# Optimization experiments

Hardware: AMD Instinct MI355X
Metric: run time of the kernel (lower is better)

Reference implementation:

```python
import jax, jax.numpy as jnp
import numpy as np

BN_EPS = 1e-5

def setup_inputs() -> dict:
    key = jax.random.key(0)
    ks = jax.random.split(key, 13)
    bs, ch, hei, wei = 4, 32, 32, 128  # n_features = wei = 128, ch = n_features//4
    nf = wei
    def p(k, shape, s=0.05):
        return jax.random.normal(k, shape, dtype=jnp.float32) * s
    return {
        "head": jax.random.normal(ks[0], (bs, ch, hei, wei), dtype=jnp.float32),
        "tail": jax.random.normal(ks[1], (bs, ch, hei, wei), dtype=jnp.float32),
        "R_q": p(ks[2], (nf, nf)), "R_k": p(ks[3], (nf, nf)),
        "R_v": p(ks[4], (nf, nf)), "R_W": p(ks[5], (nf, nf)),
        "F_q": p(ks[6], (nf, nf)), "F_k": p(ks[7], (nf, nf)),
        "F_v": p(ks[8], (nf, nf)), "F_W": p(ks[9], (nf, nf)),
        "conv_w": p(ks[10], (2, 2 * ch, 1, 1)),
        "conv_b": jnp.zeros((2,), jnp.float32),
        "bn_w": jnp.ones((2,), jnp.float32),
        "bn_b": jnp.zeros((2,), jnp.float32),
        "bn_mean": jnp.zeros((2,), jnp.float32),
        "bn_var": jnp.ones((2,), jnp.float32),
        "flag": 1,
    }

def _affinity(head, tail, conv_w, conv_b, bn_w, bn_b, bn_mean, bn_var):
    # 1x1 conv -> eval-mode BatchNorm2d -> ReLU -> softmax over channel dim
    x = jnp.concatenate([head, tail], axis=1)                       # [b,2c,h,w]
    a = jnp.einsum('bchw,oc->bohw', x, conv_w[:, :, 0, 0]) + conv_b[None, :, None, None]
    scale = (bn_w / jnp.sqrt(bn_var + BN_EPS))[None, :, None, None]
    a = (a - bn_mean[None, :, None, None]) * scale + bn_b[None, :, None, None]
    a = jax.nn.relu(a)
    return jax.nn.softmax(a, axis=1)                                # torch legacy dim=1 for 4D

def reference(head, tail, R_q, R_k, R_v, R_W, F_q, F_k, F_v, F_W,
              conv_w, conv_b, bn_w, bn_b, bn_mean, bn_var, flag):
    bs, ch, hei, wei = head.shape
    L = hei * wei
    ic = ch  # inter_channels == ch by construction
    aff = _affinity(head, tail, conv_w, conv_b, bn_w, bn_b, bn_mean, bn_var)
    if flag:
        alpha = aff[:, 0].reshape(bs, L, 1)                          # broadcast over last axis
        q = (head @ R_q).reshape(bs, ic, L).transpose(0, 2, 1)       # [b,L,ic]
        t_k = (tail @ F_k).reshape(bs, ic, L).transpose(0, 2, 1)     # [b,L,ic]
        t_v = (tail @ F_v).reshape(bs, ic, L)                        # [b,ic,L]
        f_t = t_k @ t_v                                              # [b,L,L]
        h_k = (head @ R_k).reshape(bs, ic, L).transpose(0, 2, 1)
        h_v = (head @ R_v).reshape(bs, ic, L)
        f_h = h_k @ h_v                                              # [b,L,L]
        att = jax.nn.softmax(alpha * f_t + f_h, axis=-1)
        y = (att @ q).transpose(0, 2, 1).reshape(bs, ic, hei, wei)
        return y @ R_W + head
    else:
        alpha = aff[:, 1].reshape(bs, L, 1)
        q = (tail @ F_q).reshape(bs, ic, L).transpose(0, 2, 1)
        h_k = (head @ R_k).reshape(bs, ic, L).transpose(0, 2, 1)
        h_v = (head @ R_v).reshape(bs, ic, L)
        f_h = h_k @ h_v
        t_k = (tail @ F_k).reshape(bs, ic, L).transpose(0, 2, 1)
        t_v = (tail @ F_v).reshape(bs, ic, L)
        f_t = t_k @ t_v
        att = jax.nn.softmax(alpha * f_h + f_t, axis=-1)
        y = (att @ q).transpose(0, 2, 1).reshape(bs, ic, hei, wei)
        return y @ F_W + tail
```

## Files before the change

### kernel.cpp

```cpp
#include <hip/hip_runtime.h>
#include <hip/hip_bf16.h>
#include <stdint.h>

typedef unsigned short u16;
typedef unsigned int u32;
typedef __attribute__((ext_vector_type(8))) short short8;
typedef __attribute__((ext_vector_type(4))) short short4_t;
typedef __attribute__((ext_vector_type(4))) float f32x4;

#define MFMA16(A,B,C) __builtin_amdgcn_mfma_f32_16x16x32_bf16((A),(B),(C),0,0,0)
#define L2E 1.4426950408889634f

__device__ __forceinline__ u16 f2bf(float f) {
  u32 x = __float_as_uint(f);
  u32 r = x + 0x7fffu + ((x >> 16) & 1u);
  return (u16)(r >> 16);
}
__device__ __forceinline__ float bf2f(short v) {
  return __uint_as_float((u32)(u16)v << 16);
}
__device__ __forceinline__ u32 pack_bf2(float a, float b) {
  __hip_bfloat162 h = __float22bfloat162_rn(make_float2(a, b));
  u32 u; __builtin_memcpy(&u, &h, 4); return u;
}
__device__ __forceinline__ short8 mk_frag(u32 w0, u32 w1, u32 w2, u32 w3) {
  union { u32 u[4]; short8 s; } cv;
  cv.u[0] = w0; cv.u[1] = w1; cv.u[2] = w2; cv.u[3] = w3;
  return cv.s;
}

__global__ void kprep(const float* R_q, const float* R_k, const float* R_v,
                      const float* R_W, const float* F_q, const float* F_k,
                      const float* F_v, const float* F_W, const int* flagp,
                      u16* matT)
{
  int flag = *flagp;
  const float* S;
  int m = blockIdx.x;
  if (flag) {
    const float* s[6] = {R_q, R_k, R_v, F_k, F_v, R_W}; S = s[m];
  } else {
    const float* s[6] = {F_q, F_k, F_v, R_k, R_v, F_W}; S = s[m];
  }
  u16* dst = matT + m * 16384;
  int base = blockIdx.y * 2048;
  for (int idx = base + threadIdx.x; idx < base + 2048; idx += blockDim.x) {
    int k = idx >> 7, n = idx & 127;
    dst[n * 128 + k] = f2bf(S[idx]);
  }
}

__global__ __launch_bounds__(256) void kproj(const float* __restrict__ head,
    const float* __restrict__ tail, const u16* __restrict__ matT,
    const float* __restrict__ conv_w, const float* __restrict__ conv_b,
    const float* __restrict__ bn_w, const float* __restrict__ bn_b,
    const float* __restrict__ bn_mean, const float* __restrict__ bn_var,
    u16* __restrict__ qT, u16* __restrict__ KQ,
    u16* __restrict__ Vc, const int* __restrict__ flagp)
{
  __shared__ u16 lds_t[128][34];
  __shared__ float s_alpha[128];
  const int flag = *flagp;
  const float* X1 = flag ? head : tail;
  const float* X2 = flag ? tail : head;
  const int bh = blockIdx.x, g = blockIdx.y;
  const int b = bh >> 5, h = bh & 31;
  const float* src = (g < 3) ? X1 : X2;
  const u16* Bm = matT + g * 16384;
  const int tid = threadIdx.x, lane = tid & 63, wid = tid >> 6;
  const int lrow = lane & 15, lg = lane >> 4;
  const int rt = wid & 1, cbase = (wid >> 1) * 64;

  if (g == 3) {
    if (tid < 128) {
      int w = tid;
      const float* hp = head + ((size_t)b * 1024 + h) * 128 + w;
      const float* tp = tail + ((size_t)b * 1024 + h) * 128 + w;
      float a0 = 0.f, a1 = 0.f;
      for (int c = 0; c < 32; ++c) {
        float xh = hp[c * 4096];
        float xt = tp[c * 4096];
        a0 += xh * conv_w[c]      + xt * conv_w[32 + c];
        a1 += xh * conv_w[64 + c] + xt * conv_w[96 + c];
      }
      const float eps = 1e-5f;
      a0 += conv_b[0]; a1 += conv_b[1];
      a0 = (a0 - bn_mean[0]) * (bn_w[0] * rsqrtf(bn_var[0] + eps)) + bn_b[0];
      a1 = (a1 - bn_mean[1]) * (bn_w[1] * rsqrtf(bn_var[1] + eps)) + bn_b[1];
      a0 = fmaxf(a0, 0.f); a1 = fmaxf(a1, 0.f);
      float asel = flag ? a0 : a1, aoth = flag ? a1 : a0;
      s_alpha[w] = 1.f / (1.f + __expf(aoth - asel));
    }
    __syncthreads();
  }

  f32x4 acc[4] = {};
  const float* Arow = src + (((size_t)b * 32 + rt * 16 + lrow) * 32 + h) * 128;
  #pragma unroll
  for (int k0 = 0; k0 < 128; k0 += 32) {
    short8 af;
    const float* ap = Arow + k0 + lg * 8;
    #pragma unroll
    for (int j = 0; j < 8; ++j) af[j] = (short)f2bf(ap[j]);
    #pragma unroll
    for (int cc = 0; cc < 4; ++cc) {
      short8 bf = *reinterpret_cast<const short8*>(
          Bm + (cbase + cc * 16 + lrow) * 128 + k0 + lg * 8);
      acc[cc] = MFMA16(af, bf, acc[cc]);
    }
  }
  #pragma unroll
  for (int cc = 0; cc < 4; ++cc) {
    int n = cbase + cc * 16 + lrow;
    float asc = (g == 1) ? L2E : 1.f;
    if (g == 3) asc = s_alpha[n] * L2E;
    #pragma unroll
    for (int rr = 0; rr < 4; ++rr) {
      int c = rt * 16 + lg * 4 + rr;
      lds_t[n][c] = f2bf(acc[cc][rr] * asc);
    }
  }
  __syncthreads();
  if (g == 0) {
    int c = tid >> 3, w0 = (tid & 7) * 16;
    int tw[8];
    #pragma unroll
    for (int i2 = 0; i2 < 8; ++i2)
      tw[i2] = (int)lds_t[w0 + 2 * i2][c] | ((int)lds_t[w0 + 2 * i2 + 1][c] << 16);
    int4* dst = reinterpret_cast<int4*>(qT + ((size_t)b * 32 + c) * 4096 + h * 128 + w0);
    dst[0] = make_int4(tw[0], tw[1], tw[2], tw[3]);
    dst[1] = make_int4(tw[4], tw[5], tw[6], tw[7]);
  } else if (tid < 128) {
    int w = tid;
    int tw[16];
    #pragma unroll
    for (int i2 = 0; i2 < 16; ++i2)
      tw[i2] = (int)lds_t[w][2 * i2] | ((int)lds_t[w][2 * i2 + 1] << 16);
    u16* base = (g == 2 || g == 4) ? Vc : KQ;
    int coff = (g >= 3) ? 32 : 0;
    int4* dst = reinterpret_cast<int4*>(base + ((size_t)b * 4096 + h * 128 + w) * 64 + coff);
    dst[0] = make_int4(tw[0],  tw[1],  tw[2],  tw[3]);
    dst[1] = make_int4(tw[4],  tw[5],  tw[6],  tw[7]);
    dst[2] = make_int4(tw[8],  tw[9],  tw[10], tw[11]);
    dst[3] = make_int4(tw[12], tw[13], tw[14], tw[15]);
  }
}

__global__ __launch_bounds__(256, 6) void kattn(const u16* __restrict__ qT,
    const u16* __restrict__ KQ, const u16* __restrict__ Vc,
    u16* __restrict__ pO, float* __restrict__ pm, float* __restrict__ pl)
{
  __shared__ __align__(16) char lds_v[2][8192];
  __shared__ __align__(16) char lds_q[2][4096];
  const int b = blockIdx.y;
  const int i0 = blockIdx.x * 64;
  const int sp = blockIdx.z;
  const int jbase = sp * 512;
  const int tid = threadIdx.x, lane = tid & 63, wid = tid >> 6;
  const int lrow = lane & 15, lg = lane >> 4;

  const u16* KQb = KQ + (size_t)b * 4096 * 64;
  const u16* Vb  = Vc + (size_t)b * 4096 * 64;
  const u16* qTb = qT + (size_t)b * 32 * 4096;

  short8 bkq[2];
  {
    int r = i0 + wid * 16 + lrow;
    #pragma unroll
    for (int kc = 0; kc < 2; ++kc)
      bkq[kc] = *reinterpret_cast<const short8*>(KQb + (size_t)r * 64 + kc * 32 + lg * 8);
  }

  const int sr = tid >> 3, sx = (tid & 7) * 16;
  const int pr = (((sr >> 2) & 3) << 3) + (((sr >> 4) & 1) << 2) + (sr & 3);

  #pragma unroll
  for (int q = 0; q < 2; ++q) {
    int r = sr + q * 32, gr = pr + q * 32;
    int4 v = *reinterpret_cast<const int4*>(
        reinterpret_cast<const char*>(Vb + (size_t)(jbase + gr) * 64) + sx);
    *reinterpret_cast<int4*>(lds_v[0] + r * 128 + (sx ^ ((r & 7) << 4))) = v;
  }
  {
    int4 qv = *reinterpret_cast<const int4*>(
        qTb + (size_t)sr * 4096 + jbase + (tid & 7) * 8);
    *reinterpret_cast<int4*>(lds_q[0] + sr * 128 + (sx ^ ((sr & 7) << 4))) = qv;
  }
  __syncthreads();

  float m_run = -1e30f, l_run = 0.f;
  f32x4 accO[2] = {};
  int4 stgV[2], stgQ;

  for (int t = 0; t < 8; ++t) {
    const int buf = t & 1;
    if (t < 7) {
      const u16* Vn = Vb + (size_t)(jbase + (t + 1) * 64) * 64;
      #pragma unroll
      for (int q = 0; q < 2; ++q) {
        int gr = pr + q * 32;
        stgV[q] = *reinterpret_cast<const int4*>(
            reinterpret_cast<const char*>(Vn + (size_t)gr * 64) + sx);
      }
      stgQ = *reinterpret_cast<const int4*>(
          qTb + (size_t)sr * 4096 + jbase + (t + 1) * 64 + (tid & 7) * 8);
    }
    f32x4 st[4];
    __builtin_amdgcn_s_setprio(1);
    #pragma unroll
    for (int sub = 0; sub < 4; ++sub) {
      f32x4 a = {};
      #pragma unroll
      for (int kc = 0; kc < 2; ++kc) {
        int r = sub * 16 + lrow;
        int xs = kc * 64 + lg * 16;
        short8 av = *reinterpret_cast<const short8*>(
            lds_v[buf] + r * 128 + (xs ^ ((r & 7) << 4)));
        a = MFMA16(av, bkq[kc], a);
      }
      st[sub] = a;
    }
    __builtin_amdgcn_s_setprio(0);
    short8 aq[2][2];
    #pragma unroll
    for (int w = 0; w < 2; ++w)
      #pragma unroll
      for (int ct = 0; ct < 2; ++ct) {
        int r = ct * 16 + lrow;
        int xs = w * 64 + lg * 16;
        aq[w][ct] = *reinterpret_cast<const short8*>(
            lds_q[buf] + r * 128 + (xs ^ ((r & 7) << 4)));
      }
    float tm = -1e30f;
    #pragma unroll
    for (int sub = 0; sub < 4; ++sub)
      #pragma unroll
      for (int rr = 0; rr < 4; ++rr) tm = fmaxf(tm, st[sub][rr]);
    tm = fmaxf(tm, __shfl_xor(tm, 16, 64));
    tm = fmaxf(tm, __shfl_xor(tm, 32, 64));
    if (!__all((int)(tm <= m_run + 8.f))) {
      float m_new = fmaxf(m_run, tm);
      float scale = exp2f(m_run - m_new);
      l_run *= scale;
      #pragma unroll
      for (int ct = 0; ct < 2; ++ct)
        #pragma unroll
        for (int rr = 0; rr < 4; ++rr) accO[ct][rr] *= scale;
      m_run = m_new;
    }
    float ps = 0.f;
    #pragma unroll
    for (int sub = 0; sub < 4; ++sub)
      #pragma unroll
      for (int rr = 0; rr < 4; ++rr) {
        float p = exp2f(st[sub][rr] - m_run);
        st[sub][rr] = p;
        ps += p;
      }
    ps += __shfl_xor(ps, 16, 64);
    ps += __shfl_xor(ps, 32, 64);
    l_run += ps;

    __builtin_amdgcn_s_setprio(1);
    #pragma unroll
    for (int w = 0; w < 2; ++w) {
      short8 bp = mk_frag(pack_bf2(st[2 * w][0],     st[2 * w][1]),
                          pack_bf2(st[2 * w][2],     st[2 * w][3]),
                          pack_bf2(st[2 * w + 1][0], st[2 * w + 1][1]),
                          pack_bf2(st[2 * w + 1][2], st[2 * w + 1][3]));
      #pragma unroll
      for (int ct = 0; ct < 2; ++ct)
        accO[ct] = MFMA16(aq[w][ct], bp, accO[ct]);
    }
    __builtin_amdgcn_s_setprio(0);

    if (t < 7) {
      #pragma unroll
      for (int q = 0; q < 2; ++q) {
        int r = sr + q * 32;
        *reinterpret_cast<int4*>(lds_v[buf ^ 1] + r * 128 + (sx ^ ((r & 7) << 4))) = stgV[q];
      }
      *reinterpret_cast<int4*>(lds_q[buf ^ 1] + sr * 128 + (sx ^ ((sr & 7) << 4))) = stgQ;
      __syncthreads();
    }
  }

  const int i = i0 + wid * 16 + lrow;
  u16* pOb = pO + (size_t)((b * 8 + sp) * 32) * 4096;
  #pragma unroll
  for (int ct = 0; ct < 2; ++ct)
    #pragma unroll
    for (int rr = 0; rr < 4; ++rr)
      pOb[(size_t)(ct * 16 + lg * 4 + rr) * 4096 + i] = f2bf(accO[ct][rr]);
  if (lg == 0) {
    pm[(b * 8 + sp) * 4096 + i] = m_run;
    pl[(b * 8 + sp) * 4096 + i] = l_run;
  }
}

__global__ __launch_bounds__(128) void kout(const u16* __restrict__ pO,
    const float* __restrict__ pm, const float* __restrict__ pl,
    const u16* __restrict__ matT, const float* __restrict__ head,
    const float* __restrict__ tail, const int* __restrict__ flagp,
    float* __restrict__ out)
{
  __shared__ u16 ylds[16][136];
  const int flag = *flagp;
  const float* X1 = flag ? head : tail;
  const u16* Bm = matT + 5 * 16384;
  const int tid = threadIdx.x;
  const int rbase = blockIdx.x * 16;
  const int b = rbase >> 10, c = (rbase >> 5) & 31, h0 = rbase & 31;
  const int ioff = h0 * 128 + tid * 16;

  #pragma unroll
  for (int iq = 0; iq < 4; ++iq) {
    float4 msp[8];
    #pragma unroll
    for (int sp = 0; sp < 8; ++sp)
      msp[sp] = *reinterpret_cast<const float4*>(
          pm + (size_t)((b * 8 + sp) * 4096) + ioff + iq * 4);
    float4 M4 = msp[0];
    #pragma unroll
    for (int sp = 1; sp < 8; ++sp) {
      M4.x = fmaxf(M4.x, msp[sp].x); M4.y = fmaxf(M4.y, msp[sp].y);
      M4.z = fmaxf(M4.z, msp[sp].z); M4.w = fmaxf(M4.w, msp[sp].w);
    }
    float4 L4 = {0.f, 0.f, 0.f, 0.f}, y4 = {0.f, 0.f, 0.f, 0.f};
    #pragma unroll
    for (int sp = 0; sp < 8; ++sp) {
      float4 w4;
      w4.x = exp2f(msp[sp].x - M4.x); w4.y = exp2f(msp[sp].y - M4.y);
      w4.z = exp2f(msp[sp].z - M4.z); w4.w = exp2f(msp[sp].w - M4.w);
      float4 l4 = *reinterpret_cast<const float4*>(
          pl + (size_t)((b * 8 + sp) * 4096) + ioff + iq * 4);
      L4.x += w4.x * l4.x; L4.y += w4.y * l4.y;
      L4.z += w4.z * l4.z; L4.w += w4.w * l4.w;
      short4_t o4 = *reinterpret_cast<const short4_t*>(
          pO + (size_t)(((b * 8 + sp) * 32 + c)) * 4096 + ioff + iq * 4);
      y4.x += w4.x * bf2f(o4[0]); y4.y += w4.y * bf2f(o4[1]);
      y4.z += w4.z * bf2f(o4[2]); y4.w += w4.w * bf2f(o4[3]);
    }
    y4.x /= L4.x; y4.y /= L4.y; y4.z /= L4.z; y4.w /= L4.w;
    uint2 pk2;
    pk2.x = pack_bf2(y4.x, y4.y);
    pk2.y = pack_bf2(y4.z, y4.w);
    *reinterpret_cast<uint2*>(&ylds[tid >> 3][(tid & 7) * 16 + iq * 4]) = pk2;
  }
  __syncthreads();

  const int lane = tid & 63, wid = tid >> 6;
  const int lrow = lane & 15, lg = lane >> 4;
  const int ctbase = wid * 4;
  f32x4 acc[4] = {};
  #pragma unroll
  for (int k0 = 0; k0 < 128; k0 += 32) {
    short8 af = *reinterpret_cast<const short8*>(&ylds[lrow][k0 + lg * 8]);
    #pragma unroll
    for (int cc = 0; cc < 4; ++cc) {
      short8 bf = *reinterpret_cast<const short8*>(
          Bm + (size_t)((ctbase + cc) * 16 + lrow) * 128 + k0 + lg * 8);
      acc[cc] = MFMA16(af, bf, acc[cc]);
    }
  }
  #pragma unroll
  for (int cc = 0; cc < 4; ++cc)
    #pragma unroll
    for (int rr = 0; rr < 4; ++rr) {
      int row = rbase + lg * 4 + rr;
      int col = (ctbase + cc) * 16 + lrow;
      size_t idx = (size_t)row * 128 + col;
      out[idx] = acc[cc][rr] + X1[idx];
    }
}

extern "C" void kernel_launch(void* const* d_in, const int* in_sizes, int n_in,
                              void* d_out, int out_size, void* d_ws, size_t ws_size,
                              hipStream_t stream)
{
  const float* head    = (const float*)d_in[0];
  const float* tail    = (const float*)d_in[1];
  const float* R_q     = (const float*)d_in[2];
  const float* R_k     = (const float*)d_in[3];
  const float* R_v     = (const float*)d_in[4];
  const float* R_W     = (const float*)d_in[5];
  const float* F_q     = (const float*)d_in[6];
  const float* F_k     = (const float*)d_in[7];
  const float* F_v     = (const float*)d_in[8];
  const float* F_W     = (const float*)d_in[9];
  const float* conv_w  = (const float*)d_in[10];
  const float* conv_b  = (const float*)d_in[11];
  const float* bn_w    = (const float*)d_in[12];
  const float* bn_b    = (const float*)d_in[13];
  const float* bn_mean = (const float*)d_in[14];
  const float* bn_var  = (const float*)d_in[15];
  const int*   flagp   = (const int*)d_in[16];
  float* out = (float*)d_out;

  char* ws = (char*)d_ws;
  u16*   matT = (u16*)(ws);
  u16*   qT   = (u16*)(ws + 262144);
  u16*   KQ   = (u16*)(ws + 1310720);
  u16*   Vc   = (u16*)(ws + 3407872);
  u16*   pO   = (u16*)(ws + 6553600);
  float* pm   = (float*)(ws + 14942208);
  float* pl   = (float*)(ws + 15466496);

  kprep <<<dim3(6, 8), 256, 0, stream>>>(R_q, R_k, R_v, R_W, F_q, F_k, F_v, F_W, flagp, matT);
  kproj <<<dim3(128, 5), 256, 0, stream>>>(head, tail, matT, conv_w, conv_b,
                                           bn_w, bn_b, bn_mean, bn_var,
                                           qT, KQ, Vc, flagp);
  kattn <<<dim3(64, 4, 8), 256, 0, stream>>>(qT, KQ, Vc, pO, pm, pl);
  kout  <<<256, 128, 0, stream>>>(pO, pm, pl, matT, head, tail, flagp, out);
}
```

Measured before the change: 63.08 us.

## Vectorize projection loads, use permlane reductions, and enlarge output-kernel blocks

In the projection kernel, the A-fragment now comes from two float4 loads packed with the bf16 pair conversion, replacing eight scalar loads and conversions. In the attention softmax, row max and sum use tree reductions and permlane16/32 swap builtins, when the compiler provides them, in place of shuffle-xor. The output kernel processes 32 rows per 256-thread block instead of 16 rows per 128-thread block, halving the grid and splitting the 128x128 GEMM into 2x2 wave tiles. The aim is fewer instructions in the hot softmax loop and fewer, fuller blocks in the final kernel, at the cost of less grid parallelism in kout.

```diff
diff --git a/kernel.cpp b/kernel.cpp
--- a/kernel.cpp
+++ b/kernel.cpp
@@ -28,6 +28,40 @@
   cv.u[0] = w0; cv.u[1] = w1; cv.u[2] = w2; cv.u[3] = w3;
   return cv.s;
 }
+__device__ __forceinline__ float vmax4(f32x4 v) {
+  return fmaxf(fmaxf(v[0], v[1]), fmaxf(v[2], v[3]));
+}
+__device__ __forceinline__ float vsum4(f32x4 v) {
+  return (v[0] + v[1]) + (v[2] + v[3]);
+}
+
+#if __has_builtin(__builtin_amdgcn_permlane16_swap) && __has_builtin(__builtin_amdgcn_permlane32_swap)
+__device__ __forceinline__ float quad_max16(float x) {
+  u32 xu = __float_as_uint(x);
+  auto a = __builtin_amdgcn_permlane16_swap(xu, xu, false, false);
+  float m = fmaxf(__uint_as_float(a[0]), __uint_as_float(a[1]));
+  u32 mu = __float_as_uint(m);
+  auto b = __builtin_amdgcn_permlane32_swap(mu, mu, false, false);
+  return fmaxf(__uint_as_float(b[0]), __uint_as_float(b[1]));
+}
+__device__ __forceinline__ float quad_sum16(float x) {
+  u32 xu = __float_as_uint(x);
+  auto a = __builtin_amdgcn_permlane16_swap(xu, xu, false, false);
+  float m = __uint_as_float(a[0]) + __uint_as_float(a[1]);
+  u32 mu = __float_as_uint(m);
+  auto b = __builtin_amdgcn_permlane32_swap(mu, mu, false, false);
+  return __uint_as_float(b[0]) + __uint_as_float(b[1]);
+}
+#else
+__device__ __forceinline__ float quad_max16(float x) {
+  x = fmaxf(x, __shfl_xor(x, 16, 64));
+  return fmaxf(x, __shfl_xor(x, 32, 64));
+}
+__device__ __forceinline__ float quad_sum16(float x) {
+  x += __shfl_xor(x, 16, 64);
+  return x + __shfl_xor(x, 32, 64);
+}
+#endif
 
 __global__ void kprep(const float* R_q, const float* R_k, const float* R_v,
                       const float* R_W, const float* F_q, const float* F_k,
@@ -98,10 +132,11 @@
   const float* Arow = src + (((size_t)b * 32 + rt * 16 + lrow) * 32 + h) * 128;
   #pragma unroll
   for (int k0 = 0; k0 < 128; k0 += 32) {
-    short8 af;
     const float* ap = Arow + k0 + lg * 8;
-    #pragma unroll
-    for (int j = 0; j < 8; ++j) af[j] = (short)f2bf(ap[j]);
+    float4 f0 = *reinterpret_cast<const float4*>(ap);
+    float4 f1 = *reinterpret_cast<const float4*>(ap + 4);
+    short8 af = mk_frag(pack_bf2(f0.x, f0.y), pack_bf2(f0.z, f0.w),
+                        pack_bf2(f1.x, f1.y), pack_bf2(f1.z, f1.w));
     #pragma unroll
     for (int cc = 0; cc < 4; ++cc) {
       short8 bf = *reinterpret_cast<const short8*>(
@@ -231,13 +266,9 @@
         aq[w][ct] = *reinterpret_cast<const short8*>(
             lds_q[buf] + r * 128 + (xs ^ ((r & 7) << 4)));
       }
-    float tm = -1e30f;
-    #pragma unroll
-    for (int sub = 0; sub < 4; ++sub)
-      #pragma unroll
-      for (int rr = 0; rr < 4; ++rr) tm = fmaxf(tm, st[sub][rr]);
-    tm = fmaxf(tm, __shfl_xor(tm, 16, 64));
-    tm = fmaxf(tm, __shfl_xor(tm, 32, 64));
+    float tm = fmaxf(fmaxf(vmax4(st[0]), vmax4(st[1])),
+                     fmaxf(vmax4(st[2]), vmax4(st[3])));
+    tm = quad_max16(tm);
     if (!__all((int)(tm <= m_run + 8.f))) {
       float m_new = fmaxf(m_run, tm);
       float scale = exp2f(m_run - m_new);
@@ -248,18 +279,13 @@
         for (int rr = 0; rr < 4; ++rr) accO[ct][rr] *= scale;
       m_run = m_new;
     }
-    float ps = 0.f;
     #pragma unroll
     for (int sub = 0; sub < 4; ++sub)
       #pragma unroll
-      for (int rr = 0; rr < 4; ++rr) {
-        float p = exp2f(st[sub][rr] - m_run);
-        st[sub][rr] = p;
-        ps += p;
-      }
-    ps += __shfl_xor(ps, 16, 64);
-    ps += __shfl_xor(ps, 32, 64);
-    l_run += ps;
+      for (int rr = 0; rr < 4; ++rr)
+        st[sub][rr] = exp2f(st[sub][rr] - m_run);
+    float ps = (vsum4(st[0]) + vsum4(st[1])) + (vsum4(st[2]) + vsum4(st[3]));
+    l_run += quad_sum16(ps);
 
     __builtin_amdgcn_s_setprio(1);
     #pragma unroll
@@ -298,20 +324,20 @@
   }
 }
 
-__global__ __launch_bounds__(128) void kout(const u16* __restrict__ pO,
+__global__ __launch_bounds__(256) void kout(const u16* __restrict__ pO,
     const float* __restrict__ pm, const float* __restrict__ pl,
     const u16* __restrict__ matT, const float* __restrict__ head,
     const float* __restrict__ tail, const int* __restrict__ flagp,
     float* __restrict__ out)
 {
-  __shared__ u16 ylds[16][136];
+  __shared__ u16 ylds[32][136];
   const int flag = *flagp;
   const float* X1 = flag ? head : tail;
   const u16* Bm = matT + 5 * 16384;
   const int tid = threadIdx.x;
-  const int rbase = blockIdx.x * 16;
-  const int b = rbase >> 10, c = (rbase >> 5) & 31, h0 = rbase & 31;
-  const int ioff = h0 * 128 + tid * 16;
+  const int b = blockIdx.x >> 5, c = blockIdx.x & 31;
+  const int rbase = blockIdx.x * 32;
+  const int ioff = tid * 16;
 
   #pragma unroll
   for (int iq = 0; iq < 4; ++iq) {
@@ -351,15 +377,15 @@
 
   const int lane = tid & 63, wid = tid >> 6;
   const int lrow = lane & 15, lg = lane >> 4;
-  const int ctbase = wid * 4;
+  const int rg = (wid & 1) * 16, cg = (wid >> 1) * 64;
   f32x4 acc[4] = {};
   #pragma unroll
   for (int k0 = 0; k0 < 128; k0 += 32) {
-    short8 af = *reinterpret_cast<const short8*>(&ylds[lrow][k0 + lg * 8]);
+    short8 af = *reinterpret_cast<const short8*>(&ylds[rg + lrow][k0 + lg * 8]);
     #pragma unroll
     for (int cc = 0; cc < 4; ++cc) {
       short8 bf = *reinterpret_cast<const short8*>(
-          Bm + (size_t)((ctbase + cc) * 16 + lrow) * 128 + k0 + lg * 8);
+          Bm + (size_t)(cg + cc * 16 + lrow) * 128 + k0 + lg * 8);
       acc[cc] = MFMA16(af, bf, acc[cc]);
     }
   }
@@ -367,8 +393,8 @@
   for (int cc = 0; cc < 4; ++cc)
     #pragma unroll
     for (int rr = 0; rr < 4; ++rr) {
-      int row = rbase + lg * 4 + rr;
-      int col = (ctbase + cc) * 16 + lrow;
+      int row = rbase + rg + lg * 4 + rr;
+      int col = cg + cc * 16 + lrow;
       size_t idx = (size_t)row * 128 + col;
       out[idx] = acc[cc][rr] + X1[idx];
     }
@@ -411,5 +437,5 @@
                                            bn_w, bn_b, bn_mean, bn_var,
                                            qT, KQ, Vc, flagp);
   kattn <<<dim3(64, 4, 8), 256, 0, stream>>>(qT, KQ, Vc, pO, pm, pl);
-  kout  <<<256, 128, 0, stream>>>(pO, pm, pl, matT, head, tail, flagp, out);
-}
+  kout  <<<128, 256, 0, stream>>>(pO, pm, pl, matT, head, tail, flagp, out);
+}
```

New measurement: 66.28 us. 5.1% more time.
